# Optimization experiments

Hardware: AMD Instinct MI355X
Metric: run time of the kernel (lower is better)

## Reference

```python
import jax, jax.numpy as jnp
import numpy as np

N_WRD = 2000
WCODE = 3
EMB = 32
VSIZE = 7
VIEW = (16, 16)
B = 64
CSIZE = 128


def _vcode():
    # torch.meshgrid with default 'ij' indexing, cat -> (2, H*W) -> (H*W, 2)
    x = jnp.linspace(-1.0, 1.0, VIEW[0])
    y = jnp.linspace(-1.0, 1.0, VIEW[1])
    xg, yg = jnp.meshgrid(x, y, indexing='ij')
    return jnp.stack([xg.reshape(-1), yg.reshape(-1)], axis=-1)  # (V, 2)


def setup_inputs() -> dict:
    key = jax.random.key(0)
    ks = jax.random.split(key, 20)
    s = 0.02
    d = {
        'view_cell': jax.random.normal(ks[0], (B, CSIZE, VIEW[0] * VIEW[1]), jnp.float32),
        'v': jax.random.normal(ks[1], (B, VSIZE), jnp.float32),
        'w2c_w1': jax.random.normal(ks[2], (VSIZE, 512), jnp.float32) * s,
        'w2c_b1': jnp.zeros((512,), jnp.float32),
        'w2c_w2': jax.random.normal(ks[3], (512, WCODE * N_WRD), jnp.float32) * s,
        'w2c_b2': jnp.zeros((WCODE * N_WRD,), jnp.float32),
        'fc1_w': jax.random.normal(ks[4], (WCODE, 256), jnp.float32) * s,
        'fc1_b': jnp.zeros((256,), jnp.float32),
        'fc2_w': jax.random.normal(ks[5], (256, 256), jnp.float32) * s,
        'fc2_b': jnp.zeros((256,), jnp.float32),
        'fca_w': jax.random.normal(ks[6], (256, 1), jnp.float32) * s,
        'fca_b': jnp.zeros((1,), jnp.float32),
        'fce_w': jax.random.normal(ks[7], (256, EMB), jnp.float32) * s,
        'fce_b': jnp.zeros((EMB,), jnp.float32),
        'vse_w1': jax.random.normal(ks[8], (2, 128), jnp.float32) * s,
        'vse_b1': jnp.zeros((128,), jnp.float32),
        'vse_w2': jax.random.normal(ks[9], (128, EMB), jnp.float32) * s,
        'vse_b2': jnp.zeros((EMB,), jnp.float32),
    }
    return d


def reference(view_cell, v, w2c_w1, w2c_b1, w2c_w2, w2c_b2,
              fc1_w, fc1_b, fc2_w, fc2_b, fca_w, fca_b, fce_w, fce_b,
              vse_w1, vse_b1, vse_w2, vse_b2):
    b = v.shape[0]
    # w2c: v -> per-cell world codes
    h0 = jax.nn.relu(v @ w2c_w1 + w2c_b1)                     # (B, 512)
    wcode = (h0 @ w2c_w2 + w2c_b2).reshape(-1, WCODE)          # (B*N, 3)
    h = jax.nn.relu(wcode @ fc1_w + fc1_b)                     # (B*N, 256)
    h = jax.nn.relu(h @ fc2_w + fc2_b)
    activation = jax.nn.sigmoid(h @ fca_w + fca_b).reshape(b, N_WRD, 1)
    cs_emb = (h @ fce_w + fce_b).reshape(b, N_WRD, EMB)        # (B, N, E)
    # view-space embedding of the pixel grid
    vcode = _vcode()                                           # (V, 2)
    vs = jax.nn.relu(vcode @ vse_w1 + vse_b1) @ vse_w2 + vse_b2  # (V, E)
    # relation / gated softmax routing
    relation = jnp.einsum('bne,ve->bnv', cs_emb, vs)           # (B, N, V)
    route = jax.nn.softmax(relation, axis=2) * activation      # (B, N, V)
    # write: view_cell (B, C, V) @ route^T (B, V, N) -> (B, C, N)
    wrd_cell = jnp.einsum('bcv,bnv->bcn', view_cell, route)
    return wrd_cell
```

## Files before the change

kernel.cpp:

```cpp
#include <hip/hip_runtime.h>
#include <hip/hip_bf16.h>
#include <math.h>

#define NWRD 2000
#define BB 64
#define CS 128
#define VV 256

typedef __attribute__((ext_vector_type(8)))  short short8;
typedef __attribute__((ext_vector_type(16))) float f32x16;

#define WS_FC2WT 0
#define WS_WCODE (WS_FC2WT + 32768)
#define WS_VSB   (WS_WCODE + 384000)
#define WS_W2T   (WS_VSB + 4096)
#define WS_VCB   (WS_W2T + 1536000)
#define WS_FCEWT (WS_VCB + 1048576)
#define WS_H0B   (WS_FCEWT + 4096)
#define WS_FCAWB (WS_H0B + 16384)

__device__ __forceinline__ unsigned short f2bf(float x) {
    unsigned int u = __float_as_uint(x);
    u += 0x7fffu + ((u >> 16) & 1u);
    return (unsigned short)(u >> 16);
}
__device__ __forceinline__ unsigned int pkbf(float lo, float hi) {
    unsigned int r;
    asm("v_cvt_pk_bf16_f32 %0, %1, %2" : "=v"(r) : "v"(lo), "v"(hi));
    return r;
}

#define PR_K2  94
#define PR_VCB (PR_K2 + 1024)
#define PR_VSB (PR_VCB + 32)
#define PR_FC2 (PR_VSB + 16)
#define PREP_N (PR_FC2 + 1)
__global__ __launch_bounds__(256) void kprep(
        const float* __restrict__ vc, unsigned short* __restrict__ vcb,
        const float* __restrict__ w2,
        const float* __restrict__ v, const float* __restrict__ w1,
        const float* __restrict__ b1, const float* __restrict__ b2,
        float* __restrict__ wcode,
        const float* __restrict__ vse_w1, const float* __restrict__ vse_b1,
        const float* __restrict__ vse_w2, const float* __restrict__ vse_b2,
        unsigned short* __restrict__ vsb,
        const float* __restrict__ fc2_w, unsigned short* __restrict__ fc2wT,
        const float* __restrict__ fce_w, unsigned short* __restrict__ fcewT,
        const float* __restrict__ fca_w, unsigned short* __restrict__ fcawB) {
    __shared__ __align__(16) unsigned short smem[9216];
    int bid = blockIdx.x, t = threadIdx.x;
    if (bid < PR_K2) {
        unsigned short* ha = smem;
        unsigned short* wb = smem + 4608;
        int n0 = bid * 64;
        int w = t >> 6, lane = t & 63, l31 = lane & 31, h = lane >> 5;
        int mt = w & 1, nt = w >> 1;
        int kk = t & 63, mg = t >> 6;
        int colc = n0 + kk; if (colc > 5999) colc = 5999;
        f32x16 acc;
#pragma unroll
        for (int i = 0; i < 16; i++) acc[i] = 0.f;
        for (int p = 0; p < 8; p++) {
            int k0 = p * 64;
            float w1c[7];
#pragma unroll
            for (int q = 0; q < 7; q++) w1c[q] = w1[q*512 + k0 + kk];
            float bbv = b1[k0 + kk];
#pragma unroll
            for (int mm = 0; mm < 16; mm++) {
                int m = mg*16 + mm;
                float s = bbv;
#pragma unroll
                for (int q = 0; q < 7; q++) s = fmaf(v[m*7 + q], w1c[q], s);
                ha[m*72 + kk] = f2bf(fmaxf(s, 0.f));
            }
#pragma unroll
            for (int i = 0; i < 16; i++)
                wb[kk*72 + mg*16 + i] = f2bf(w2[(size_t)(k0 + mg*16 + i)*6000 + colc]);
            __syncthreads();
#pragma unroll
            for (int ks = 0; ks < 4; ks++) {
                short8 af = *(const short8*)(ha + (mt*32 + l31)*72 + ks*16 + h*8);
                short8 bf = *(const short8*)(wb + (nt*32 + l31)*72 + ks*16 + h*8);
                acc = __builtin_amdgcn_mfma_f32_32x32x16_bf16(af, bf, acc, 0, 0, 0);
            }
            __syncthreads();
        }
        int n = n0 + nt*32 + l31;
        if (n < 6000) {
            float bias = b2[n];
#pragma unroll
            for (int i = 0; i < 16; i++) {
                int row = (i & 3) + 8*(i >> 2) + 4*h;
                wcode[(size_t)(mt*32 + row)*6000 + n] = acc[i] + bias;
            }
        }
    } else if (bid < PR_VCB) {
        int i = ((bid - PR_K2) * 256 + t) * 8;
        float4 f0 = *(const float4*)(vc + i);
        float4 f1 = *(const float4*)(vc + i + 4);
        union { short8 v8; unsigned int u[4]; } o;
        o.u[0] = pkbf(f0.x, f0.y); o.u[1] = pkbf(f0.z, f0.w);
        o.u[2] = pkbf(f1.x, f1.y); o.u[3] = pkbf(f1.z, f1.w);
        *(short8*)(vcb + i) = o.v8;
    } else if (bid < PR_VSB) {
        float* hs = (float*)smem;
        int blk = bid - PR_VCB;
        int m = t & 127, half = t >> 7;
#pragma unroll
        for (int q = 0; q < 4; q++) {
            int vloc = half*4 + q;
            int vv = blk*8 + vloc;
            float x = (2.f/15.f)*(float)(vv >> 4) - 1.f;
            float y = (2.f/15.f)*(float)(vv & 15) - 1.f;
            float hh = vse_b1[m] + x*vse_w1[m] + y*vse_w1[128 + m];
            hs[vloc*128 + m] = fmaxf(hh, 0.f);
        }
        __syncthreads();
        int vloc = t >> 5, e = t & 31;
        float s = vse_b2[e];
        for (int mm = 0; mm < 128; mm++) s = fmaf(hs[vloc*128 + mm], vse_w2[mm*32 + e], s);
        vsb[(blk*8 + vloc)*32 + e] = f2bf(s);
    } else if (bid < PR_FC2) {
        unsigned short (*tile)[72] = (unsigned short(*)[72])smem;
        int b2t = bid - PR_VSB;
        int k0t = (b2t >> 2) * 64, n0t = (b2t & 3) * 64;
        int nl = t & 63, kb = (t >> 6) * 16;
#pragma unroll
        for (int i = 0; i < 16; i++)
            tile[kb + i][nl] = f2bf(fc2_w[(size_t)(k0t + kb + i)*256 + n0t + nl]);
        __syncthreads();
        int kl = t & 63, nb = (t >> 6) * 16;
#pragma unroll
        for (int i = 0; i < 16; i++)
            fc2wT[(size_t)(n0t + nb + i)*256 + k0t + kl] = tile[kl][nb + i];
    } else {
        int e = t & 31, kb = (t >> 5) * 32;
        unsigned short tmp[32];
#pragma unroll
        for (int i = 0; i < 32; i++) tmp[i] = f2bf(fce_w[(size_t)(kb + i)*32 + e]);
#pragma unroll
        for (int i = 0; i < 4; i++)
            *(short8*)(fcewT + (size_t)e*256 + kb + i*8) = *(short8*)(tmp + i*8);
#pragma unroll
        for (int i = 0; i < 32; i++)
            fcawB[(size_t)e*256 + kb + i] = (e == 0) ? f2bf(fca_w[kb + i]) : (unsigned short)0;
    }
}

#define K45_LDS 77056
__global__ __launch_bounds__(512, 4) void k45(
        const unsigned short* __restrict__ vcb,
        const float* __restrict__ wcode,
        const float* __restrict__ fc1_w, const float* __restrict__ fc1_b,
        const unsigned short* __restrict__ fc2wT, const float* __restrict__ fc2_b,
        const float* __restrict__ fca_b_p,
        const unsigned short* __restrict__ fcawB,
        const unsigned short* __restrict__ fcewT, const float* __restrict__ fce_b,
        const unsigned short* __restrict__ vsb,
        float* __restrict__ out) {
    extern __shared__ char lds[];
    unsigned short* h1b    = (unsigned short*)lds;
    unsigned short* h2b    = (unsigned short*)(lds + 33792);
    unsigned short* routeB = h2b;
    unsigned short* embL   = (unsigned short*)(lds + 67584);
    float* actL   = (float*)(lds + 72704);
    float* wcsAll = (float*)(lds + 72960);
    float* redS   = (float*)(lds + 76032);
    int t = threadIdx.x;
    int w = t >> 6, lane = t & 63, l31 = lane & 31, h = lane >> 5;
    int b = blockIdx.y;
    int n0 = blockIdx.x * 256;

    {
        const float* wb = wcode + (size_t)b*6000;
        int i0 = n0*3 + t;
        wcsAll[t] = wb[i0 < 6000 ? i0 : 5999];
        if (t < 256) {
            int i1 = n0*3 + 512 + t;
            wcsAll[512 + t] = wb[i1 < 6000 ? i1 : 5999];
        }
    }
    int jq = (t & 63) * 4;
    float4 wa  = *(const float4*)(fc1_w + jq);
    float4 wb4 = *(const float4*)(fc1_w + 256 + jq);
    float4 wc  = *(const float4*)(fc1_w + 512 + jq);
    float4 bb4 = *(const float4*)(fc1_b + jq);
    int nW = w*32 + l31;
    float b2v = fc2_b[nW];
    float be = fce_b[l31];
    float fcab = fca_b_p[0];
    int ntR = w & 1, vq = w >> 1;
    int ctE = w >> 1, ntE = w & 1;
    size_t arowE = ((size_t)(b*128 + ctE*32 + l31))*256;
    __syncthreads();

    for (int c = 0; c < 4; c++) {
        int w0 = n0 + c*64;
#pragma unroll
        for (int rr = 0; rr < 8; rr++) {
            int r = w*8 + rr;
            const float* wr = wcsAll + (c*64 + r)*3;
            float c0 = wr[0], c1 = wr[1], c2 = wr[2];
            float v0 = fmaxf(fmaf(c2, wc.x, fmaf(c1, wb4.x, fmaf(c0, wa.x, bb4.x))), 0.f);
            float v1 = fmaxf(fmaf(c2, wc.y, fmaf(c1, wb4.y, fmaf(c0, wa.y, bb4.y))), 0.f);
            float v2 = fmaxf(fmaf(c2, wc.z, fmaf(c1, wb4.z, fmaf(c0, wa.z, bb4.z))), 0.f);
            float v3 = fmaxf(fmaf(c2, wc.w, fmaf(c1, wb4.w, fmaf(c0, wa.w, bb4.w))), 0.f);
            uint2 p;
            p.x = pkbf(v0, v1);
            p.y = pkbf(v2, v3);
            *(uint2*)(h1b + r*264 + jq) = p;
        }
        __syncthreads();
        {
            f32x16 c0, c1;
#pragma unroll
            for (int i = 0; i < 16; i++) { c0[i] = 0.f; c1[i] = 0.f; }
#pragma unroll 4
            for (int ks = 0; ks < 16; ks++) {
                int k0 = ks*16 + h*8;
                short8 bf  = *(const short8*)(fc2wT + (size_t)nW*256 + k0);
                short8 af0 = *(const short8*)(h1b + l31*264 + k0);
                short8 af1 = *(const short8*)(h1b + (32 + l31)*264 + k0);
                c0 = __builtin_amdgcn_mfma_f32_32x32x16_bf16(af0, bf, c0, 0, 0, 0);
                c1 = __builtin_amdgcn_mfma_f32_32x32x16_bf16(af1, bf, c1, 0, 0, 0);
            }
#pragma unroll
            for (int i = 0; i < 16; i++) {
                int row = (i & 3) + 8*(i >> 2) + 4*h;
                unsigned int pk = pkbf(fmaxf(c0[i] + b2v, 0.f), fmaxf(c1[i] + b2v, 0.f));
                h2b[row*264 + nW]        = (unsigned short)pk;
                h2b[(row + 32)*264 + nW] = (unsigned short)(pk >> 16);
            }
        }
        __syncthreads();
        if (w < 2) {
            f32x16 ce;
#pragma unroll
            for (int i = 0; i < 16; i++) ce[i] = 0.f;
#pragma unroll 4
            for (int ks = 0; ks < 16; ks++) {
                int k0 = ks*16 + h*8;
                short8 af = *(const short8*)(h2b + (w*32 + l31)*264 + k0);
                short8 bf = *(const short8*)(fcewT + (size_t)l31*256 + k0);
                ce = __builtin_amdgcn_mfma_f32_32x32x16_bf16(af, bf, ce, 0, 0, 0);
            }
#pragma unroll
            for (int i = 0; i < 16; i += 2) {
                int row = (i & 3) + 8*(i >> 2) + 4*h;
                unsigned int pk = pkbf(ce[i] + be, ce[i+1] + be);
                embL[(w*32 + row)*40 + l31]     = (unsigned short)pk;
                embL[(w*32 + row + 1)*40 + l31] = (unsigned short)(pk >> 16);
            }
        } else if (w < 4) {
            int m = w - 2;
            f32x16 ca;
#pragma unroll
            for (int i = 0; i < 16; i++) ca[i] = 0.f;
#pragma unroll 4
            for (int ks = 0; ks < 16; ks++) {
                int k0 = ks*16 + h*8;
                short8 af = *(const short8*)(h2b + (m*32 + l31)*264 + k0);
                short8 bf = *(const short8*)(fcawB + (size_t)l31*256 + k0);
                ca = __builtin_amdgcn_mfma_f32_32x32x16_bf16(af, bf, ca, 0, 0, 0);
            }
            if (l31 == 0) {
#pragma unroll
                for (int i = 0; i < 16; i++) {
                    int row = (i & 3) + 8*(i >> 2) + 4*h;
                    actL[m*32 + row] = 1.f / (1.f + __expf(-(ca[i] + fcab)));
                }
            }
        }
        __syncthreads();
        int nloc = ntR*32 + l31;
        f32x16 ra[2];
#pragma unroll
        for (int mt = 0; mt < 2; mt++)
#pragma unroll
            for (int i = 0; i < 16; i++) ra[mt][i] = 0.f;
#pragma unroll
        for (int s = 0; s < 2; s++) {
            short8 bfrag = *(const short8*)(embL + nloc*40 + s*16 + h*8);
#pragma unroll
            for (int mt = 0; mt < 2; mt++) {
                int vrow = (vq*2 + mt)*32 + l31;
                short8 afrag = *(const short8*)(vsb + vrow*32 + s*16 + h*8);
                ra[mt] = __builtin_amdgcn_mfma_f32_32x32x16_bf16(afrag, bfrag, ra[mt], 0, 0, 0);
            }
        }
        float sm = 0.f;
#pragma unroll
        for (int mt = 0; mt < 2; mt++)
#pragma unroll
            for (int i = 0; i < 16; i++) {
                float e = __expf(ra[mt][i]);
                ra[mt][i] = e;
                sm += e;
            }
        sm += __shfl_xor(sm, 32);
        if (lane < 32) redS[w*32 + l31] = sm;
        __syncthreads();
        sm = 0.f;
#pragma unroll
        for (int q = 0; q < 4; q++) sm += redS[(q*2 + ntR)*32 + l31];
        float scale = actL[nloc] / sm;
#pragma unroll
        for (int mt = 0; mt < 2; mt++) {
#pragma unroll
            for (int rp = 0; rp < 4; rp++) {
                int vb = (vq*2 + mt)*32 + rp*8 + h*4;
                unsigned int p0 = pkbf(ra[mt][rp*4+0]*scale, ra[mt][rp*4+1]*scale);
                unsigned int p1 = pkbf(ra[mt][rp*4+2]*scale, ra[mt][rp*4+3]*scale);
                *(uint2*)(routeB + nloc*264 + vb) = make_uint2(p0, p1);
            }
        }
        __syncthreads();
        {
            f32x16 cc;
#pragma unroll
            for (int i = 0; i < 16; i++) cc[i] = 0.f;
            const unsigned short* rrow = routeB + (ntE*32 + l31)*264;
#pragma unroll 4
            for (int ks = 0; ks < 16; ks++) {
                int k0 = ks*16 + h*8;
                short8 bf = *(const short8*)(rrow + k0);
                short8 a0 = *(const short8*)(vcb + arowE + k0);
                cc = __builtin_amdgcn_mfma_f32_32x32x16_bf16(a0, bf, cc, 0, 0, 0);
            }
            int ng = w0 + ntE*32 + l31;
            if (ng < NWRD) {
                float* ob = out + (size_t)b*128*NWRD + ng;
#pragma unroll
                for (int i = 0; i < 16; i++) {
                    int crow = (i & 3) + 8*(i >> 2) + 4*h;
                    ob[(size_t)(ctE*32 + crow)*NWRD] = cc[i];
                }
            }
        }
    }
}

extern "C" void kernel_launch(void* const* d_in, const int* in_sizes, int n_in,
                              void* d_out, int out_size, void* d_ws, size_t ws_size,
                              hipStream_t stream) {
    const float* view_cell = (const float*)d_in[0];
    const float* v       = (const float*)d_in[1];
    const float* w2c_w1  = (const float*)d_in[2];
    const float* w2c_b1  = (const float*)d_in[3];
    const float* w2c_w2  = (const float*)d_in[4];
    const float* w2c_b2  = (const float*)d_in[5];
    const float* fc1_w   = (const float*)d_in[6];
    const float* fc1_b   = (const float*)d_in[7];
    const float* fc2_w   = (const float*)d_in[8];
    const float* fc2_b   = (const float*)d_in[9];
    const float* fca_w   = (const float*)d_in[10];
    const float* fca_b   = (const float*)d_in[11];
    const float* fce_w   = (const float*)d_in[12];
    const float* fce_b   = (const float*)d_in[13];
    const float* vse_w1  = (const float*)d_in[14];
    const float* vse_b1  = (const float*)d_in[15];
    const float* vse_w2  = (const float*)d_in[16];
    const float* vse_b2  = (const float*)d_in[17];
    float* ws    = (float*)d_ws;
    unsigned short* fc2wT = (unsigned short*)(ws + WS_FC2WT);
    float* wcode = ws + WS_WCODE;
    unsigned short* vsb   = (unsigned short*)(ws + WS_VSB);
    unsigned short* vcb   = (unsigned short*)(ws + WS_VCB);
    unsigned short* fcewT = (unsigned short*)(ws + WS_FCEWT);
    unsigned short* fcawB = (unsigned short*)(ws + WS_FCAWB);
    float* out   = (float*)d_out;

    kprep<<<PREP_N, 256, 0, stream>>>(view_cell, vcb,
                                      w2c_w2, v, w2c_w1, w2c_b1, w2c_b2, wcode,
                                      vse_w1, vse_b1, vse_w2, vse_b2, vsb,
                                      fc2_w, fc2wT, fce_w, fcewT, fca_w, fcawB);
    (void)hipFuncSetAttribute((const void*)k45,
                              hipFuncAttributeMaxDynamicSharedMemorySize, K45_LDS);
    dim3 g45(8, 64);
    k45<<<g45, 512, K45_LDS, stream>>>(vcb, wcode, fc1_w, fc1_b, fc2wT, fc2_b,
                                       fca_b, fcawB, fcewT, fce_b, vsb, out);
}
```

Baseline: 204.1 us.

## Fold fce projection into view embedding and shrink k45 tiles for occupancy

```diff
diff --git a/kernel.cpp b/kernel.cpp
--- a/kernel.cpp
+++ b/kernel.cpp
@@ -3,9 +3,6 @@
 #include <math.h>
 
 #define NWRD 2000
-#define BB 64
-#define CS 128
-#define VV 256
 
 typedef __attribute__((ext_vector_type(8)))  short short8;
 typedef __attribute__((ext_vector_type(16))) float f32x16;
@@ -32,8 +29,8 @@
 
 #define PR_K2  94
 #define PR_VCB (PR_K2 + 1024)
-#define PR_VSB (PR_VCB + 32)
-#define PR_FC2 (PR_VSB + 16)
+#define PR_VF  (PR_VCB + 8)
+#define PR_FC2 (PR_VF + 16)
 #define PREP_N (PR_FC2 + 1)
 __global__ __launch_bounds__(256) void kprep(
         const float* __restrict__ vc, unsigned short* __restrict__ vcb,
@@ -43,11 +40,11 @@
         float* __restrict__ wcode,
         const float* __restrict__ vse_w1, const float* __restrict__ vse_b1,
         const float* __restrict__ vse_w2, const float* __restrict__ vse_b2,
-        unsigned short* __restrict__ vsb,
+        const float* __restrict__ fce_w, const float* __restrict__ fce_b,
+        unsigned short* __restrict__ vfb, float* __restrict__ rbuf,
         const float* __restrict__ fc2_w, unsigned short* __restrict__ fc2wT,
-        const float* __restrict__ fce_w, unsigned short* __restrict__ fcewT,
         const float* __restrict__ fca_w, unsigned short* __restrict__ fcawB) {
-    __shared__ __align__(16) unsigned short smem[9216];
+    __shared__ __align__(16) unsigned short smem[10240];
     int bid = blockIdx.x, t = threadIdx.x;
     if (bid < PR_K2) {
         unsigned short* ha = smem;
@@ -103,27 +100,49 @@
         o.u[0] = pkbf(f0.x, f0.y); o.u[1] = pkbf(f0.z, f0.w);
         o.u[2] = pkbf(f1.x, f1.y); o.u[3] = pkbf(f1.z, f1.w);
         *(short8*)(vcb + i) = o.v8;
-    } else if (bid < PR_VSB) {
-        float* hs = (float*)smem;
+    } else if (bid < PR_VF) {
+        float* hs  = (float*)smem;
+        float* vsf = hs + 4096;
         int blk = bid - PR_VCB;
-        int m = t & 127, half = t >> 7;
-#pragma unroll
-        for (int q = 0; q < 4; q++) {
-            int vloc = half*4 + q;
-            int vv = blk*8 + vloc;
+        int v0 = blk * 32;
+#pragma unroll
+        for (int q = 0; q < 16; q++) {
+            int idx = q*256 + t;
+            int vloc = idx >> 7, m = idx & 127;
+            int vv = v0 + vloc;
             float x = (2.f/15.f)*(float)(vv >> 4) - 1.f;
             float y = (2.f/15.f)*(float)(vv & 15) - 1.f;
-            float hh = vse_b1[m] + x*vse_w1[m] + y*vse_w1[128 + m];
-            hs[vloc*128 + m] = fmaxf(hh, 0.f);
-        }
-        __syncthreads();
-        int vloc = t >> 5, e = t & 31;
-        float s = vse_b2[e];
-        for (int mm = 0; mm < 128; mm++) s = fmaf(hs[vloc*128 + mm], vse_w2[mm*32 + e], s);
-        vsb[(blk*8 + vloc)*32 + e] = f2bf(s);
+            hs[vloc*128 + m] = fmaxf(vse_b1[m] + x*vse_w1[m] + y*vse_w1[128 + m], 0.f);
+        }
+        __syncthreads();
+#pragma unroll
+        for (int q = 0; q < 4; q++) {
+            int idx = q*256 + t;
+            int vloc = idx >> 5, e = idx & 31;
+            float s = vse_b2[e];
+            for (int m = 0; m < 128; m++) s = fmaf(hs[vloc*128 + m], vse_w2[m*32 + e], s);
+            vsf[vloc*32 + e] = s;
+        }
+        __syncthreads();
+        {
+            int vloc = t >> 3, kb = (t & 7) * 32;
+            for (int j = 0; j < 32; j++) {
+                int k = kb + j;
+                float s = 0.f;
+#pragma unroll
+                for (int e = 0; e < 32; e++) s = fmaf(vsf[vloc*32 + e], fce_w[(size_t)k*32 + e], s);
+                vfb[(size_t)(v0 + vloc)*256 + k] = f2bf(s);
+            }
+            if (t < 32) {
+                float s = 0.f;
+#pragma unroll
+                for (int e = 0; e < 32; e++) s = fmaf(vsf[t*32 + e], fce_b[e], s);
+                rbuf[v0 + t] = s;
+            }
+        }
     } else if (bid < PR_FC2) {
         unsigned short (*tile)[72] = (unsigned short(*)[72])smem;
-        int b2t = bid - PR_VSB;
+        int b2t = bid - PR_VF;
         int k0t = (b2t >> 2) * 64, n0t = (b2t & 3) * 64;
         int nl = t & 63, kb = (t >> 6) * 16;
 #pragma unroll
@@ -136,208 +155,174 @@
             fc2wT[(size_t)(n0t + nb + i)*256 + k0t + kl] = tile[kl][nb + i];
     } else {
         int e = t & 31, kb = (t >> 5) * 32;
-        unsigned short tmp[32];
-#pragma unroll
-        for (int i = 0; i < 32; i++) tmp[i] = f2bf(fce_w[(size_t)(kb + i)*32 + e]);
-#pragma unroll
-        for (int i = 0; i < 4; i++)
-            *(short8*)(fcewT + (size_t)e*256 + kb + i*8) = *(short8*)(tmp + i*8);
 #pragma unroll
         for (int i = 0; i < 32; i++)
             fcawB[(size_t)e*256 + kb + i] = (e == 0) ? f2bf(fca_w[kb + i]) : (unsigned short)0;
     }
 }
 
-#define K45_LDS 77056
-__global__ __launch_bounds__(512, 4) void k45(
+#define K45_LDS 36608
+__device__ __forceinline__ void fc1_row(const float* __restrict__ wr,
+        const float4& wa, const float4& wb4, const float4& wc, const float4& bb4,
+        unsigned short* dst) {
+    float c0 = wr[0], c1 = wr[1], c2 = wr[2];
+    float v0 = fmaxf(fmaf(c2, wc.x, fmaf(c1, wb4.x, fmaf(c0, wa.x, bb4.x))), 0.f);
+    float v1 = fmaxf(fmaf(c2, wc.y, fmaf(c1, wb4.y, fmaf(c0, wa.y, bb4.y))), 0.f);
+    float v2 = fmaxf(fmaf(c2, wc.z, fmaf(c1, wb4.z, fmaf(c0, wa.z, bb4.z))), 0.f);
+    float v3 = fmaxf(fmaf(c2, wc.w, fmaf(c1, wb4.w, fmaf(c0, wa.w, bb4.w))), 0.f);
+    uint2 p;
+    p.x = pkbf(v0, v1);
+    p.y = pkbf(v2, v3);
+    *(uint2*)dst = p;
+}
+__global__ __launch_bounds__(512, 8) void k45(
         const unsigned short* __restrict__ vcb,
         const float* __restrict__ wcode,
         const float* __restrict__ fc1_w, const float* __restrict__ fc1_b,
         const unsigned short* __restrict__ fc2wT, const float* __restrict__ fc2_b,
         const float* __restrict__ fca_b_p,
         const unsigned short* __restrict__ fcawB,
-        const unsigned short* __restrict__ fcewT, const float* __restrict__ fce_b,
-        const unsigned short* __restrict__ vsb,
+        const unsigned short* __restrict__ vfb, const float* __restrict__ rbuf,
         float* __restrict__ out) {
     extern __shared__ char lds[];
     unsigned short* h1b    = (unsigned short*)lds;
-    unsigned short* h2b    = (unsigned short*)(lds + 33792);
+    unsigned short* h2b    = (unsigned short*)(lds + 16896);
     unsigned short* routeB = h2b;
-    unsigned short* embL   = (unsigned short*)(lds + 67584);
-    float* actL   = (float*)(lds + 72704);
-    float* wcsAll = (float*)(lds + 72960);
-    float* redS   = (float*)(lds + 76032);
+    float* wcsAll = (float*)(lds + 33792);
+    float* actP   = (float*)(lds + 35328);
+    float* redS   = (float*)(lds + 35584);
     int t = threadIdx.x;
     int w = t >> 6, lane = t & 63, l31 = lane & 31, h = lane >> 5;
     int b = blockIdx.y;
-    int n0 = blockIdx.x * 256;
-
-    {
-        const float* wb = wcode + (size_t)b*6000;
+    int n0 = blockIdx.x * 128;
+
+    if (t < 384) {
         int i0 = n0*3 + t;
-        wcsAll[t] = wb[i0 < 6000 ? i0 : 5999];
-        if (t < 256) {
-            int i1 = n0*3 + 512 + t;
-            wcsAll[512 + t] = wb[i1 < 6000 ? i1 : 5999];
-        }
+        wcsAll[t] = wcode[(size_t)b*6000 + (i0 < 6000 ? i0 : 5999)];
     }
-    int jq = (t & 63) * 4;
-    float4 wa  = *(const float4*)(fc1_w + jq);
-    float4 wb4 = *(const float4*)(fc1_w + 256 + jq);
-    float4 wc  = *(const float4*)(fc1_w + 512 + jq);
-    float4 bb4 = *(const float4*)(fc1_b + jq);
     int nW = w*32 + l31;
     float b2v = fc2_b[nW];
-    float be = fce_b[l31];
     float fcab = fca_b_p[0];
-    int ntR = w & 1, vq = w >> 1;
-    int ctE = w >> 1, ntE = w & 1;
-    size_t arowE = ((size_t)(b*128 + ctE*32 + l31))*256;
+    size_t arowE = ((size_t)(b*128 + (w & 3)*32 + l31))*256;
     __syncthreads();
 
+    {
+        int jq = (t & 63) * 4;
+        float4 wa  = *(const float4*)(fc1_w + jq);
+        float4 wb4 = *(const float4*)(fc1_w + 256 + jq);
+        float4 wc  = *(const float4*)(fc1_w + 512 + jq);
+        float4 bb4 = *(const float4*)(fc1_b + jq);
+        int rbase = (t >> 6) * 4;
+#pragma unroll
+        for (int rr = 0; rr < 4; rr++) {
+            int r = rbase + rr;
+            fc1_row(wcsAll + r*3, wa, wb4, wc, bb4, h1b + r*264 + jq);
+        }
+    }
+    __syncthreads();
+
     for (int c = 0; c < 4; c++) {
-        int w0 = n0 + c*64;
-#pragma unroll
-        for (int rr = 0; rr < 8; rr++) {
-            int r = w*8 + rr;
-            const float* wr = wcsAll + (c*64 + r)*3;
-            float c0 = wr[0], c1 = wr[1], c2 = wr[2];
-            float v0 = fmaxf(fmaf(c2, wc.x, fmaf(c1, wb4.x, fmaf(c0, wa.x, bb4.x))), 0.f);
-            float v1 = fmaxf(fmaf(c2, wc.y, fmaf(c1, wb4.y, fmaf(c0, wa.y, bb4.y))), 0.f);
-            float v2 = fmaxf(fmaf(c2, wc.z, fmaf(c1, wb4.z, fmaf(c0, wa.z, bb4.z))), 0.f);
-            float v3 = fmaxf(fmaf(c2, wc.w, fmaf(c1, wb4.w, fmaf(c0, wa.w, bb4.w))), 0.f);
-            uint2 p;
-            p.x = pkbf(v0, v1);
-            p.y = pkbf(v2, v3);
-            *(uint2*)(h1b + r*264 + jq) = p;
-        }
-        __syncthreads();
         {
-            f32x16 c0, c1;
-#pragma unroll
-            for (int i = 0; i < 16; i++) { c0[i] = 0.f; c1[i] = 0.f; }
+            f32x16 acc;
+#pragma unroll
+            for (int i = 0; i < 16; i++) acc[i] = 0.f;
 #pragma unroll 4
             for (int ks = 0; ks < 16; ks++) {
                 int k0 = ks*16 + h*8;
-                short8 bf  = *(const short8*)(fc2wT + (size_t)nW*256 + k0);
-                short8 af0 = *(const short8*)(h1b + l31*264 + k0);
-                short8 af1 = *(const short8*)(h1b + (32 + l31)*264 + k0);
-                c0 = __builtin_amdgcn_mfma_f32_32x32x16_bf16(af0, bf, c0, 0, 0, 0);
-                c1 = __builtin_amdgcn_mfma_f32_32x32x16_bf16(af1, bf, c1, 0, 0, 0);
+                short8 af = *(const short8*)(h1b + l31*264 + k0);
+                short8 bf = *(const short8*)(fc2wT + (size_t)nW*256 + k0);
+                acc = __builtin_amdgcn_mfma_f32_32x32x16_bf16(af, bf, acc, 0, 0, 0);
             }
 #pragma unroll
             for (int i = 0; i < 16; i++) {
                 int row = (i & 3) + 8*(i >> 2) + 4*h;
-                unsigned int pk = pkbf(fmaxf(c0[i] + b2v, 0.f), fmaxf(c1[i] + b2v, 0.f));
-                h2b[row*264 + nW]        = (unsigned short)pk;
-                h2b[(row + 32)*264 + nW] = (unsigned short)(pk >> 16);
-            }
-        }
-        __syncthreads();
-        if (w < 2) {
-            f32x16 ce;
-#pragma unroll
-            for (int i = 0; i < 16; i++) ce[i] = 0.f;
+                h2b[row*264 + nW] = f2bf(fmaxf(acc[i] + b2v, 0.f));
+            }
+        }
+        __syncthreads();
+        if (w >= 6) {
+            f32x16 ca;
+#pragma unroll
+            for (int i = 0; i < 16; i++) ca[i] = 0.f;
+            int ksb = (w == 6) ? 0 : 8;
+#pragma unroll
+            for (int ks = 0; ks < 8; ks++) {
+                int k0 = (ksb + ks)*16 + h*8;
+                short8 af = *(const short8*)(fcawB + (size_t)l31*256 + k0);
+                short8 bf = *(const short8*)(h2b + l31*264 + k0);
+                ca = __builtin_amdgcn_mfma_f32_32x32x16_bf16(af, bf, ca, 0, 0, 0);
+            }
+            if (lane < 32) actP[(w - 6)*32 + l31] = ca[0];
+        }
+        f32x16 ra;
+#pragma unroll
+        for (int i = 0; i < 16; i++) ra[i] = 0.f;
+#pragma unroll 4
+        for (int ks = 0; ks < 16; ks++) {
+            int k0 = ks*16 + h*8;
+            short8 af = *(const short8*)(vfb + (size_t)(w*32 + l31)*256 + k0);
+            short8 bf = *(const short8*)(h2b + l31*264 + k0);
+            ra = __builtin_amdgcn_mfma_f32_32x32x16_bf16(af, bf, ra, 0, 0, 0);
+        }
+        float sm = 0.f;
+#pragma unroll
+        for (int i = 0; i < 16; i++) {
+            int row = (i & 3) + 8*(i >> 2) + 4*h;
+            float e = __expf(ra[i] + rbuf[w*32 + row]);
+            ra[i] = e;
+            sm += e;
+        }
+        sm += __shfl_xor(sm, 32);
+        if (lane < 32) redS[w*32 + l31] = sm;
+        __syncthreads();
+        float smt = 0.f;
+#pragma unroll
+        for (int q = 0; q < 8; q++) smt += redS[q*32 + l31];
+        float al = actP[l31] + actP[32 + l31] + fcab;
+        float scale = (1.f / (1.f + __expf(-al))) / smt;
+#pragma unroll
+        for (int g = 0; g < 4; g++) {
+            int vb = w*32 + 8*g + 4*h;
+            unsigned int p0 = pkbf(ra[g*4+0]*scale, ra[g*4+1]*scale);
+            unsigned int p1 = pkbf(ra[g*4+2]*scale, ra[g*4+3]*scale);
+            *(uint2*)(routeB + l31*264 + vb) = make_uint2(p0, p1);
+        }
+        __syncthreads();
+        if (w < 4) {
+            f32x16 cc;
+#pragma unroll
+            for (int i = 0; i < 16; i++) cc[i] = 0.f;
 #pragma unroll 4
             for (int ks = 0; ks < 16; ks++) {
                 int k0 = ks*16 + h*8;
-                short8 af = *(const short8*)(h2b + (w*32 + l31)*264 + k0);
-                short8 bf = *(const short8*)(fcewT + (size_t)l31*256 + k0);
-                ce = __builtin_amdgcn_mfma_f32_32x32x16_bf16(af, bf, ce, 0, 0, 0);
-            }
-#pragma unroll
-            for (int i = 0; i < 16; i += 2) {
-                int row = (i & 3) + 8*(i >> 2) + 4*h;
-                unsigned int pk = pkbf(ce[i] + be, ce[i+1] + be);
-                embL[(w*32 + row)*40 + l31]     = (unsigned short)pk;
-                embL[(w*32 + row + 1)*40 + l31] = (unsigned short)(pk >> 16);
-            }
-        } else if (w < 4) {
-            int m = w - 2;
-            f32x16 ca;
-#pragma unroll
-            for (int i = 0; i < 16; i++) ca[i] = 0.f;
-#pragma unroll 4
-            for (int ks = 0; ks < 16; ks++) {
-                int k0 = ks*16 + h*8;
-                short8 af = *(const short8*)(h2b + (m*32 + l31)*264 + k0);
-                short8 bf = *(const short8*)(fcawB + (size_t)l31*256 + k0);
-                ca = __builtin_amdgcn_mfma_f32_32x32x16_bf16(af, bf, ca, 0, 0, 0);
-            }
-            if (l31 == 0) {
-#pragma unroll
-                for (int i = 0; i < 16; i++) {
-                    int row = (i & 3) + 8*(i >> 2) + 4*h;
-                    actL[m*32 + row] = 1.f / (1.f + __expf(-(ca[i] + fcab)));
-                }
-            }
-        }
-        __syncthreads();
-        int nloc = ntR*32 + l31;
-        f32x16 ra[2];
-#pragma unroll
-        for (int mt = 0; mt < 2; mt++)
-#pragma unroll
-            for (int i = 0; i < 16; i++) ra[mt][i] = 0.f;
-#pragma unroll
-        for (int s = 0; s < 2; s++) {
-            short8 bfrag = *(const short8*)(embL + nloc*40 + s*16 + h*8);
-#pragma unroll
-            for (int mt = 0; mt < 2; mt++) {
-                int vrow = (vq*2 + mt)*32 + l31;
-                short8 afrag = *(const short8*)(vsb + vrow*32 + s*16 + h*8);
-                ra[mt] = __builtin_amdgcn_mfma_f32_32x32x16_bf16(afrag, bfrag, ra[mt], 0, 0, 0);
-            }
-        }
-        float sm = 0.f;
-#pragma unroll
-        for (int mt = 0; mt < 2; mt++)
-#pragma unroll
-            for (int i = 0; i < 16; i++) {
-                float e = __expf(ra[mt][i]);
-                ra[mt][i] = e;
-                sm += e;
-            }
-        sm += __shfl_xor(sm, 32);
-        if (lane < 32) redS[w*32 + l31] = sm;
-        __syncthreads();
-        sm = 0.f;
-#pragma unroll
-        for (int q = 0; q < 4; q++) sm += redS[(q*2 + ntR)*32 + l31];
-        float scale = actL[nloc] / sm;
-#pragma unroll
-        for (int mt = 0; mt < 2; mt++) {
-#pragma unroll
-            for (int rp = 0; rp < 4; rp++) {
-                int vb = (vq*2 + mt)*32 + rp*8 + h*4;
-                unsigned int p0 = pkbf(ra[mt][rp*4+0]*scale, ra[mt][rp*4+1]*scale);
-                unsigned int p1 = pkbf(ra[mt][rp*4+2]*scale, ra[mt][rp*4+3]*scale);
-                *(uint2*)(routeB + nloc*264 + vb) = make_uint2(p0, p1);
-            }
-        }
-        __syncthreads();
-        {
-            f32x16 cc;
-#pragma unroll
-            for (int i = 0; i < 16; i++) cc[i] = 0.f;
-            const unsigned short* rrow = routeB + (ntE*32 + l31)*264;
-#pragma unroll 4
-            for (int ks = 0; ks < 16; ks++) {
-                int k0 = ks*16 + h*8;
-                short8 bf = *(const short8*)(rrow + k0);
+                short8 bf = *(const short8*)(routeB + l31*264 + k0);
                 short8 a0 = *(const short8*)(vcb + arowE + k0);
                 cc = __builtin_amdgcn_mfma_f32_32x32x16_bf16(a0, bf, cc, 0, 0, 0);
             }
-            int ng = w0 + ntE*32 + l31;
+            int ng = n0 + c*32 + l31;
             if (ng < NWRD) {
                 float* ob = out + (size_t)b*128*NWRD + ng;
 #pragma unroll
                 for (int i = 0; i < 16; i++) {
                     int crow = (i & 3) + 8*(i >> 2) + 4*h;
-                    ob[(size_t)(ctE*32 + crow)*NWRD] = cc[i];
+                    ob[(size_t)(w*32 + crow)*NWRD] = cc[i];
                 }
             }
-        }
+        } else if (c < 3) {
+            int t2 = t & 255;
+            int jq = (t2 & 63) * 4;
+            float4 wa  = *(const float4*)(fc1_w + jq);
+            float4 wb4 = *(const float4*)(fc1_w + 256 + jq);
+            float4 wc  = *(const float4*)(fc1_w + 512 + jq);
+            float4 bb4 = *(const float4*)(fc1_b + jq);
+            int rbase = (t2 >> 6) * 8;
+#pragma unroll
+            for (int rr = 0; rr < 8; rr++) {
+                int r = rbase + rr;
+                fc1_row(wcsAll + ((c + 1)*32 + r)*3, wa, wb4, wc, bb4, h1b + r*264 + jq);
+            }
+        }
+        if (c < 3) __syncthreads();
     }
 }
 
@@ -365,19 +350,20 @@
     float* ws    = (float*)d_ws;
     unsigned short* fc2wT = (unsigned short*)(ws + WS_FC2WT);
     float* wcode = ws + WS_WCODE;
-    unsigned short* vsb   = (unsigned short*)(ws + WS_VSB);
+    unsigned short* vfb   = (unsigned short*)(ws + WS_W2T);
+    float* rbuf  = ws + WS_W2T + 32768;
     unsigned short* vcb   = (unsigned short*)(ws + WS_VCB);
-    unsigned short* fcewT = (unsigned short*)(ws + WS_FCEWT);
     unsigned short* fcawB = (unsigned short*)(ws + WS_FCAWB);
     float* out   = (float*)d_out;
 
     kprep<<<PREP_N, 256, 0, stream>>>(view_cell, vcb,
                                       w2c_w2, v, w2c_w1, w2c_b1, w2c_b2, wcode,
-                                      vse_w1, vse_b1, vse_w2, vse_b2, vsb,
-                                      fc2_w, fc2wT, fce_w, fcewT, fca_w, fcawB);
+                                      vse_w1, vse_b1, vse_w2, vse_b2,
+                                      fce_w, fce_b, vfb, rbuf,
+                                      fc2_w, fc2wT, fca_w, fcawB);
     (void)hipFuncSetAttribute((const void*)k45,
                               hipFuncAttributeMaxDynamicSharedMemorySize, K45_LDS);
-    dim3 g45(8, 64);
+    dim3 g45(16, 64);
     k45<<<g45, 512, K45_LDS, stream>>>(vcb, wcode, fc1_w, fc1_b, fc2wT, fc2_b,
-                                       fca_b, fcawB, fcewT, fce_b, vsb, out);
-}
+                                       fca_b, fcawB, vfb, rbuf, out);
+}
```

Result: slower. 354.2 us (+73.5%).

## Shrink k45 LDS by aliasing buffers and defer softmax scaling to the output

Applied to the files above, without the earlier changes.

```diff
diff --git a/kernel.cpp b/kernel.cpp
--- a/kernel.cpp
+++ b/kernel.cpp
@@ -3,9 +3,6 @@
 #include <math.h>
 
 #define NWRD 2000
-#define BB 64
-#define CS 128
-#define VV 256
 
 typedef __attribute__((ext_vector_type(8)))  short short8;
 typedef __attribute__((ext_vector_type(16))) float f32x16;
@@ -47,7 +44,7 @@
         const float* __restrict__ fc2_w, unsigned short* __restrict__ fc2wT,
         const float* __restrict__ fce_w, unsigned short* __restrict__ fcewT,
         const float* __restrict__ fca_w, unsigned short* __restrict__ fcawB) {
-    __shared__ __align__(16) unsigned short smem[9216];
+    __shared__ __align__(16) unsigned short smem[10240];
     int bid = blockIdx.x, t = threadIdx.x;
     if (bid < PR_K2) {
         unsigned short* ha = smem;
@@ -148,8 +145,21 @@
     }
 }
 
-#define K45_LDS 77056
-__global__ __launch_bounds__(512, 4) void k45(
+#define K45_LDS 43264
+__device__ __forceinline__ void fc1_row(const float* __restrict__ wr,
+        const float4& wa, const float4& wb4, const float4& wc, const float4& bb4,
+        unsigned short* dst) {
+    float c0 = wr[0], c1 = wr[1], c2 = wr[2];
+    float v0 = fmaxf(fmaf(c2, wc.x, fmaf(c1, wb4.x, fmaf(c0, wa.x, bb4.x))), 0.f);
+    float v1 = fmaxf(fmaf(c2, wc.y, fmaf(c1, wb4.y, fmaf(c0, wa.y, bb4.y))), 0.f);
+    float v2 = fmaxf(fmaf(c2, wc.z, fmaf(c1, wb4.z, fmaf(c0, wa.z, bb4.z))), 0.f);
+    float v3 = fmaxf(fmaf(c2, wc.w, fmaf(c1, wb4.w, fmaf(c0, wa.w, bb4.w))), 0.f);
+    uint2 p;
+    p.x = pkbf(v0, v1);
+    p.y = pkbf(v2, v3);
+    *(uint2*)dst = p;
+}
+__global__ __launch_bounds__(512, 6) void k45(
         const unsigned short* __restrict__ vcb,
         const float* __restrict__ wcode,
         const float* __restrict__ fc1_w, const float* __restrict__ fc1_b,
@@ -160,78 +170,68 @@
         const unsigned short* __restrict__ vsb,
         float* __restrict__ out) {
     extern __shared__ char lds[];
-    unsigned short* h1b    = (unsigned short*)lds;
-    unsigned short* h2b    = (unsigned short*)(lds + 33792);
-    unsigned short* routeB = h2b;
-    unsigned short* embL   = (unsigned short*)(lds + 67584);
-    float* actL   = (float*)(lds + 72704);
-    float* wcsAll = (float*)(lds + 72960);
-    float* redS   = (float*)(lds + 76032);
+    unsigned short* buf   = (unsigned short*)lds;
+    unsigned short* embL  = (unsigned short*)(lds + 33792);
+    float* wcsAll = (float*)(lds + 38912);
+    float* redS   = (float*)(lds + 41984);
+    float* actL   = (float*)(lds + 43008);
     int t = threadIdx.x;
     int w = t >> 6, lane = t & 63, l31 = lane & 31, h = lane >> 5;
     int b = blockIdx.y;
     int n0 = blockIdx.x * 256;
 
     {
-        const float* wb = wcode + (size_t)b*6000;
+        const float* wsrc = wcode + (size_t)b*6000;
         int i0 = n0*3 + t;
-        wcsAll[t] = wb[i0 < 6000 ? i0 : 5999];
+        wcsAll[t] = wsrc[i0 < 6000 ? i0 : 5999];
         if (t < 256) {
             int i1 = n0*3 + 512 + t;
-            wcsAll[512 + t] = wb[i1 < 6000 ? i1 : 5999];
+            wcsAll[512 + t] = wsrc[i1 < 6000 ? i1 : 5999];
         }
     }
     int jq = (t & 63) * 4;
-    float4 wa  = *(const float4*)(fc1_w + jq);
-    float4 wb4 = *(const float4*)(fc1_w + 256 + jq);
-    float4 wc  = *(const float4*)(fc1_w + 512 + jq);
-    float4 bb4 = *(const float4*)(fc1_b + jq);
-    int nW = w*32 + l31;
-    float b2v = fc2_b[nW];
+    int mtF = w & 1, nqF = w >> 1;
+    int colA = nqF*64 + l31, colB = colA + 32;
+    float baA = fc2_b[colA], baB = fc2_b[colB];
     float be = fce_b[l31];
     float fcab = fca_b_p[0];
     int ntR = w & 1, vq = w >> 1;
-    int ctE = w >> 1, ntE = w & 1;
-    size_t arowE = ((size_t)(b*128 + ctE*32 + l31))*256;
+    int cq = w >> 1, ntE = w & 1;
+    size_t arowE = ((size_t)(b*128 + cq*32 + l31))*256;
     __syncthreads();
 
     for (int c = 0; c < 4; c++) {
-        int w0 = n0 + c*64;
-#pragma unroll
-        for (int rr = 0; rr < 8; rr++) {
-            int r = w*8 + rr;
-            const float* wr = wcsAll + (c*64 + r)*3;
-            float c0 = wr[0], c1 = wr[1], c2 = wr[2];
-            float v0 = fmaxf(fmaf(c2, wc.x, fmaf(c1, wb4.x, fmaf(c0, wa.x, bb4.x))), 0.f);
-            float v1 = fmaxf(fmaf(c2, wc.y, fmaf(c1, wb4.y, fmaf(c0, wa.y, bb4.y))), 0.f);
-            float v2 = fmaxf(fmaf(c2, wc.z, fmaf(c1, wb4.z, fmaf(c0, wa.z, bb4.z))), 0.f);
-            float v3 = fmaxf(fmaf(c2, wc.w, fmaf(c1, wb4.w, fmaf(c0, wa.w, bb4.w))), 0.f);
-            uint2 p;
-            p.x = pkbf(v0, v1);
-            p.y = pkbf(v2, v3);
-            *(uint2*)(h1b + r*264 + jq) = p;
-        }
-        __syncthreads();
         {
-            f32x16 c0, c1;
-#pragma unroll
-            for (int i = 0; i < 16; i++) { c0[i] = 0.f; c1[i] = 0.f; }
+            float4 wa  = *(const float4*)(fc1_w + jq);
+            float4 wb4 = *(const float4*)(fc1_w + 256 + jq);
+            float4 wc  = *(const float4*)(fc1_w + 512 + jq);
+            float4 bb4 = *(const float4*)(fc1_b + jq);
+#pragma unroll
+            for (int rr = 0; rr < 8; rr++) {
+                int r = w*8 + rr;
+                fc1_row(wcsAll + (c*64 + r)*3, wa, wb4, wc, bb4, buf + r*264 + jq);
+            }
+        }
+        __syncthreads();
+        f32x16 c0, c1;
+#pragma unroll
+        for (int i = 0; i < 16; i++) { c0[i] = 0.f; c1[i] = 0.f; }
 #pragma unroll 4
-            for (int ks = 0; ks < 16; ks++) {
-                int k0 = ks*16 + h*8;
-                short8 bf  = *(const short8*)(fc2wT + (size_t)nW*256 + k0);
-                short8 af0 = *(const short8*)(h1b + l31*264 + k0);
-                short8 af1 = *(const short8*)(h1b + (32 + l31)*264 + k0);
-                c0 = __builtin_amdgcn_mfma_f32_32x32x16_bf16(af0, bf, c0, 0, 0, 0);
-                c1 = __builtin_amdgcn_mfma_f32_32x32x16_bf16(af1, bf, c1, 0, 0, 0);
-            }
-#pragma unroll
-            for (int i = 0; i < 16; i++) {
-                int row = (i & 3) + 8*(i >> 2) + 4*h;
-                unsigned int pk = pkbf(fmaxf(c0[i] + b2v, 0.f), fmaxf(c1[i] + b2v, 0.f));
-                h2b[row*264 + nW]        = (unsigned short)pk;
-                h2b[(row + 32)*264 + nW] = (unsigned short)(pk >> 16);
-            }
+        for (int ks = 0; ks < 16; ks++) {
+            int k0 = ks*16 + h*8;
+            short8 af  = *(const short8*)(buf + (mtF*32 + l31)*264 + k0);
+            short8 bf0 = *(const short8*)(fc2wT + (size_t)colA*256 + k0);
+            short8 bf1 = *(const short8*)(fc2wT + (size_t)colB*256 + k0);
+            c0 = __builtin_amdgcn_mfma_f32_32x32x16_bf16(af, bf0, c0, 0, 0, 0);
+            c1 = __builtin_amdgcn_mfma_f32_32x32x16_bf16(af, bf1, c1, 0, 0, 0);
+        }
+        __syncthreads();
+#pragma unroll
+        for (int i = 0; i < 16; i++) {
+            int row = (i & 3) + 8*(i >> 2) + 4*h;
+            unsigned int pk = pkbf(fmaxf(c0[i] + baA, 0.f), fmaxf(c1[i] + baB, 0.f));
+            buf[(mtF*32 + row)*264 + colA] = (unsigned short)pk;
+            buf[(mtF*32 + row)*264 + colB] = (unsigned short)(pk >> 16);
         }
         __syncthreads();
         if (w < 2) {
@@ -241,7 +241,7 @@
 #pragma unroll 4
             for (int ks = 0; ks < 16; ks++) {
                 int k0 = ks*16 + h*8;
-                short8 af = *(const short8*)(h2b + (w*32 + l31)*264 + k0);
+                short8 af = *(const short8*)(buf + (w*32 + l31)*264 + k0);
                 short8 bf = *(const short8*)(fcewT + (size_t)l31*256 + k0);
                 ce = __builtin_amdgcn_mfma_f32_32x32x16_bf16(af, bf, ce, 0, 0, 0);
             }
@@ -260,7 +260,7 @@
 #pragma unroll 4
             for (int ks = 0; ks < 16; ks++) {
                 int k0 = ks*16 + h*8;
-                short8 af = *(const short8*)(h2b + (m*32 + l31)*264 + k0);
+                short8 af = *(const short8*)(buf + (m*32 + l31)*264 + k0);
                 short8 bf = *(const short8*)(fcawB + (size_t)l31*256 + k0);
                 ca = __builtin_amdgcn_mfma_f32_32x32x16_bf16(af, bf, ca, 0, 0, 0);
             }
@@ -268,51 +268,48 @@
 #pragma unroll
                 for (int i = 0; i < 16; i++) {
                     int row = (i & 3) + 8*(i >> 2) + 4*h;
-                    actL[m*32 + row] = 1.f / (1.f + __expf(-(ca[i] + fcab)));
-                }
-            }
-        }
-        __syncthreads();
-        int nloc = ntR*32 + l31;
-        f32x16 ra[2];
-#pragma unroll
-        for (int mt = 0; mt < 2; mt++)
-#pragma unroll
-            for (int i = 0; i < 16; i++) ra[mt][i] = 0.f;
-#pragma unroll
-        for (int s = 0; s < 2; s++) {
-            short8 bfrag = *(const short8*)(embL + nloc*40 + s*16 + h*8);
+                    actL[m*32 + row] = ca[i];
+                }
+            }
+        }
+        __syncthreads();
+        {
+            int nloc = ntR*32 + l31;
+            f32x16 ra[2];
+#pragma unroll
+            for (int mt = 0; mt < 2; mt++)
+#pragma unroll
+                for (int i = 0; i < 16; i++) ra[mt][i] = 0.f;
+#pragma unroll
+            for (int s = 0; s < 2; s++) {
+                short8 bfrag = *(const short8*)(embL + nloc*40 + s*16 + h*8);
+#pragma unroll
+                for (int mt = 0; mt < 2; mt++) {
+                    int vrow = (vq*2 + mt)*32 + l31;
+                    short8 afrag = *(const short8*)(vsb + vrow*32 + s*16 + h*8);
+                    ra[mt] = __builtin_amdgcn_mfma_f32_32x32x16_bf16(afrag, bfrag, ra[mt], 0, 0, 0);
+                }
+            }
+            float sm = 0.f;
+#pragma unroll
+            for (int mt = 0; mt < 2; mt++)
+#pragma unroll
+                for (int i = 0; i < 16; i++) {
+                    float e = __expf(ra[mt][i]);
+                    ra[mt][i] = e;
+                    sm += e;
+                }
+            sm += __shfl_xor(sm, 32);
+            if (lane < 32) redS[w*32 + l31] = sm;
 #pragma unroll
             for (int mt = 0; mt < 2; mt++) {
-                int vrow = (vq*2 + mt)*32 + l31;
-                short8 afrag = *(const short8*)(vsb + vrow*32 + s*16 + h*8);
-                ra[mt] = __builtin_amdgcn_mfma_f32_32x32x16_bf16(afrag, bfrag, ra[mt], 0, 0, 0);
-            }
-        }
-        float sm = 0.f;
-#pragma unroll
-        for (int mt = 0; mt < 2; mt++)
-#pragma unroll
-            for (int i = 0; i < 16; i++) {
-                float e = __expf(ra[mt][i]);
-                ra[mt][i] = e;
-                sm += e;
-            }
-        sm += __shfl_xor(sm, 32);
-        if (lane < 32) redS[w*32 + l31] = sm;
-        __syncthreads();
-        sm = 0.f;
-#pragma unroll
-        for (int q = 0; q < 4; q++) sm += redS[(q*2 + ntR)*32 + l31];
-        float scale = actL[nloc] / sm;
-#pragma unroll
-        for (int mt = 0; mt < 2; mt++) {
-#pragma unroll
-            for (int rp = 0; rp < 4; rp++) {
-                int vb = (vq*2 + mt)*32 + rp*8 + h*4;
-                unsigned int p0 = pkbf(ra[mt][rp*4+0]*scale, ra[mt][rp*4+1]*scale);
-                unsigned int p1 = pkbf(ra[mt][rp*4+2]*scale, ra[mt][rp*4+3]*scale);
-                *(uint2*)(routeB + nloc*264 + vb) = make_uint2(p0, p1);
+#pragma unroll
+                for (int g = 0; g < 4; g++) {
+                    int vb = (vq*2 + mt)*32 + 8*g + 4*h;
+                    unsigned int p0 = pkbf(ra[mt][g*4+0], ra[mt][g*4+1]);
+                    unsigned int p1 = pkbf(ra[mt][g*4+2], ra[mt][g*4+3]);
+                    *(uint2*)(buf + nloc*264 + vb) = make_uint2(p0, p1);
+                }
             }
         }
         __syncthreads();
@@ -320,7 +317,7 @@
             f32x16 cc;
 #pragma unroll
             for (int i = 0; i < 16; i++) cc[i] = 0.f;
-            const unsigned short* rrow = routeB + (ntE*32 + l31)*264;
+            const unsigned short* rrow = buf + (ntE*32 + l31)*264;
 #pragma unroll 4
             for (int ks = 0; ks < 16; ks++) {
                 int k0 = ks*16 + h*8;
@@ -328,16 +325,24 @@
                 short8 a0 = *(const short8*)(vcb + arowE + k0);
                 cc = __builtin_amdgcn_mfma_f32_32x32x16_bf16(a0, bf, cc, 0, 0, 0);
             }
-            int ng = w0 + ntE*32 + l31;
+            int wloc = ntE*32 + l31;
+            float smt = 0.f;
+#pragma unroll
+            for (int q = 0; q < 4; q++) smt += redS[(q*2 + ntE)*32 + l31];
+            float al = actL[wloc] + fcab;
+            float scale = (1.f / (1.f + __expf(-al))) / smt;
+            int ng = n0 + c*64 + wloc;
             if (ng < NWRD) {
                 float* ob = out + (size_t)b*128*NWRD + ng;
 #pragma unroll
                 for (int i = 0; i < 16; i++) {
                     int crow = (i & 3) + 8*(i >> 2) + 4*h;
-                    ob[(size_t)(ctE*32 + crow)*NWRD] = cc[i];
-                }
-            }
-        }
+                    __builtin_nontemporal_store(cc[i]*scale,
+                                                ob + (size_t)(cq*32 + crow)*NWRD);
+                }
+            }
+        }
+        if (c < 3) __syncthreads();
     }
 }
 
```

New measurement: 251.2 us. +23.1%, slower.
